# Kernel tuning notes

Measured on AMD Instinct MI355X. Metric: run time of the kernel, lower is better.

## Reference

```python
import jax, jax.numpy as jnp
import numpy as np

NUM_NODES = 100_000
NUM_EDGES = 3_200_000
THETA = 1.0  # module hyperparameter (default 1.0)


def setup_inputs() -> dict:
    key = jax.random.key(0)
    k_v, k_src, k_dst, k_t1, k_t2, k_r = jax.random.split(key, 6)
    v = jax.random.normal(k_v, (NUM_NODES,), dtype=jnp.float32)
    src = jax.random.randint(k_src, (NUM_EDGES,), 0, NUM_NODES, dtype=jnp.int32)
    dst = jax.random.randint(k_dst, (NUM_EDGES,), 0, NUM_NODES, dtype=jnp.int32)
    theta_sd_1 = jax.random.normal(k_t1, (NUM_EDGES,), dtype=jnp.float32) * 0.1
    theta_sd_2 = jax.random.normal(k_t2, (NUM_EDGES,), dtype=jnp.float32) * 0.1
    # conductance = 1/resistance, resistance in (0.5, 2.0) -> conductance in (0.5, 2.0)
    conductance = 1.0 / jax.random.uniform(k_r, (NUM_EDGES,), dtype=jnp.float32, minval=0.5, maxval=2.0)
    return {"t": 0, "v": v, "src": src, "dst": dst,
            "theta_sd_1": theta_sd_1, "theta_sd_2": theta_sd_2,
            "conductance": conductance}


def reference(t, v, src, dst, theta_sd_1, theta_sd_2, conductance):
    # per-edge gated current: g(vs, vd) = relu(theta1*(vs - vd) + theta2)
    diff = v[src] - v[dst]                                   # [E]
    current = conductance * jax.nn.relu(theta_sd_1 * diff + theta_sd_2)  # [E]
    incoming = jax.ops.segment_sum(current, dst, num_segments=NUM_NODES)  # [N]
    outgoing = jax.ops.segment_sum(current, src, num_segments=NUM_NODES)  # [N]
    return (incoming - outgoing) / THETA
```

## Files before the change

kernel.cpp:

```cpp
#include <hip/hip_runtime.h>
#include <hip/hip_fp16.h>


#define TL        13
#define TILE      (1 << TL)
#define NTILES    13
#define NBINS     (NTILES * NTILES)
#define PA_BLK    1024
#define PA_EPT    4
#define PA_EPB    (PA_BLK * PA_EPT)
#define SCAPL     56
#define NREP      8
#define CURSTRIDE 16
#define PC_BLK    1024
#define S_PC      3
#define NCOPY     (2 * NTILES * S_PC)

typedef int      vi4 __attribute__((ext_vector_type(4)));
typedef float    vf4 __attribute__((ext_vector_type(4)));
typedef unsigned vu2 __attribute__((ext_vector_type(2)));

__device__ __forceinline__ unsigned f16b(float f) {
    return (unsigned)__half_as_ushort(__float2half(f));
}
__device__ __forceinline__ float f16v(unsigned u) {
    return __half2float(__ushort_as_half((unsigned short)(u & 0xFFFFu)));
}

__global__ __launch_bounds__(PA_BLK) void pa_kernel(
    const int*   __restrict__ src,
    const int*   __restrict__ dst,
    const float* __restrict__ t1,
    const float* __restrict__ t2,
    const float* __restrict__ cond,
    vu2*         __restrict__ recs,
    int*         __restrict__ cursors,
    int E, int SEGCAP)
{
    __shared__ vu2 sbuf[NBINS][SCAPL];
    __shared__ int scnt[NBINS];
    __shared__ int gbase[NBINS];

    for (int i = threadIdx.x; i < NBINS; i += PA_BLK) scnt[i] = 0;
    __syncthreads();

    const int i0 = blockIdx.x * PA_EPB + (int)threadIdx.x * PA_EPT;

    #define PUT(S, D, T1, T2, C)                                              \
        {                                                                     \
            int bin = ((S) >> TL) * NTILES + ((D) >> TL);                     \
            vu2 rec;                                                          \
            rec.x = (((unsigned)(D) & (TILE - 1)) << TL) |                    \
                    ((unsigned)(S) & (TILE - 1));                             \
            rec.y = (f16b((C) * (T1)) << 16) | f16b((C) * (T2));              \
            int idx = atomicAdd(&scnt[bin], 1);                               \
            if (idx < SCAPL) sbuf[bin][idx] = rec;                            \
        }

    if (i0 + PA_EPT <= E) {
        vi4 s4 = __builtin_nontemporal_load((const vi4*)(src  + i0));
        vi4 d4 = __builtin_nontemporal_load((const vi4*)(dst  + i0));
        vf4 a4 = __builtin_nontemporal_load((const vf4*)(t1   + i0));
        vf4 b4 = __builtin_nontemporal_load((const vf4*)(t2   + i0));
        vf4 c4 = __builtin_nontemporal_load((const vf4*)(cond + i0));
        PUT(s4.x, d4.x, a4.x, b4.x, c4.x)
        PUT(s4.y, d4.y, a4.y, b4.y, c4.y)
        PUT(s4.z, d4.z, a4.z, b4.z, c4.z)
        PUT(s4.w, d4.w, a4.w, b4.w, c4.w)
    } else {
        for (int i = i0; i < E && i < i0 + PA_EPT; ++i)
            PUT(src[i], dst[i], t1[i], t2[i], cond[i])
    }
    #undef PUT

    __syncthreads();
    const int rep = blockIdx.x & (NREP - 1);
    if (threadIdx.x < NBINS) {
        int c = min(scnt[threadIdx.x], SCAPL);
        int b = atomicAdd(&cursors[(threadIdx.x * NREP + rep) * CURSTRIDE], c);
        if (b > SEGCAP) b = SEGCAP;
        if (b + c > SEGCAP) c = SEGCAP - b;
        scnt[threadIdx.x]  = c;
        gbase[threadIdx.x] = b;
    }
    __syncthreads();

    const int wave = threadIdx.x >> 6;
    const int lane = threadIdx.x & 63;
    for (int r = wave; r < NBINS; r += (PA_BLK / 64)) {
        const int c = scnt[r];
        vu2* g = recs + (size_t)(r * NREP + rep) * SEGCAP + gbase[r];
        for (int j = lane; j < c; j += 64) g[j] = sbuf[r][j];
    }
}

__global__ __launch_bounds__(PC_BLK) void pc_kernel(
    const float* __restrict__ v,
    const vu2*   __restrict__ recs,
    const int*   __restrict__ cursors,
    float*       __restrict__ part,
    int N, int SEGCAP)
{
    __shared__ __align__(16) float tS[TILE];
    __shared__ __align__(16) float tD[TILE];
    __shared__ __align__(16) float aS[TILE];
    __shared__ __align__(16) float aD[TILE];

    const int bin = blockIdx.x / S_PC;
    const int s   = blockIdx.x % S_PC;
    const int sb  = bin / NTILES;
    const int db  = bin % NTILES;
    const int baseS = sb << TL;
    const int baseD = db << TL;
    const int lenS = min(TILE, N - baseS);
    const int lenD = min(TILE, N - baseD);

    for (int i = threadIdx.x; i < TILE; i += PC_BLK) {
        tS[i] = (i < lenS) ? v[baseS + i] : 0.0f;
        tD[i] = (i < lenD) ? v[baseD + i] : 0.0f;
        aS[i] = 0.0f;
        aD[i] = 0.0f;
    }
    __syncthreads();

    for (int rep = 0; rep < NREP; ++rep) {
        const int cnt = min(cursors[(bin * NREP + rep) * CURSTRIDE], SEGCAP);
        const int j0  = (int)((long long)cnt * s       / S_PC);
        const int j1  = (int)((long long)cnt * (s + 1) / S_PC);
        const vu2* p  = recs + (size_t)(bin * NREP + rep) * SEGCAP;
        for (int j = j0 + (int)threadIdx.x; j < j1; j += PC_BLK) {
            vu2 r = p[j];
            const int   sl = (int)(r.x & (TILE - 1));
            const int   dl = (int)((r.x >> TL) & (TILE - 1));
            const float A  = f16v(r.y >> 16);
            const float B  = f16v(r.y);
            const float x  = fmaf(A, tS[sl] - tD[dl], B);
            if (x > 0.0f) {
                atomicAdd(&aS[sl], -x);
                atomicAdd(&aD[dl],  x);
            }
        }
    }
    __syncthreads();

    if (lenS > 0) {
        float* p = part + (size_t)(db * S_PC + s) * N + baseS;
        const int l4 = lenS & ~3;
        for (int i = (int)threadIdx.x * 4; i < l4; i += PC_BLK * 4)
            *(float4*)(p + i) = *(const float4*)&aS[i];
        for (int i = l4 + (int)threadIdx.x; i < lenS; i += PC_BLK)
            p[i] = aS[i];
    }
    if (lenD > 0) {
        float* p = part + (size_t)(NTILES * S_PC + sb * S_PC + s) * N + baseD;
        const int l4 = lenD & ~3;
        for (int i = (int)threadIdx.x * 4; i < l4; i += PC_BLK * 4)
            *(float4*)(p + i) = *(const float4*)&aD[i];
        for (int i = l4 + (int)threadIdx.x; i < lenD; i += PC_BLK)
            p[i] = aD[i];
    }
}

__global__ __launch_bounds__(256) void pe_kernel(
    const float* __restrict__ part, float* __restrict__ out, int N4)
{
    int n = blockIdx.x * blockDim.x + threadIdx.x;
    if (n < N4) {
        float4 sm = make_float4(0.f, 0.f, 0.f, 0.f);
        for (int c = 0; c < NCOPY; ++c) {
            float4 q = ((const float4*)part)[(size_t)c * N4 + n];
            sm.x += q.x; sm.y += q.y; sm.z += q.z; sm.w += q.w;
        }
        ((float4*)out)[n] = sm;
    }
}

__global__ __launch_bounds__(256) void pe_scalar_kernel(
    const float* __restrict__ part, float* __restrict__ out, int N)
{
    int n = blockIdx.x * blockDim.x + threadIdx.x;
    if (n < N) {
        float sm = 0.0f;
        for (int c = 0; c < NCOPY; ++c) sm += part[(size_t)c * N + n];
        out[n] = sm;
    }
}

__global__ __launch_bounds__(256) void atomic_fallback_kernel(
    const float* __restrict__ v, const int* __restrict__ src, const int* __restrict__ dst,
    const float* __restrict__ t1, const float* __restrict__ t2, const float* __restrict__ cond,
    float* __restrict__ out, int E)
{
    int i = blockIdx.x * blockDim.x + threadIdx.x;
    int stride = gridDim.x * blockDim.x;
    for (; i < E; i += stride) {
        int s = src[i], d = dst[i];
        float x = fmaf(t1[i], v[s] - v[d], t2[i]);
        if (x > 0.0f) {
            float c = cond[i] * x;
            atomicAdd(&out[d], c);
            atomicAdd(&out[s], -c);
        }
    }
}

extern "C" void kernel_launch(void* const* d_in, const int* in_sizes, int n_in,
                              void* d_out, int out_size, void* d_ws, size_t ws_size,
                              hipStream_t stream) {
    const float* v    = (const float*)d_in[1];
    const int*   src  = (const int*)  d_in[2];
    const int*   dst  = (const int*)  d_in[3];
    const float* t1   = (const float*)d_in[4];
    const float* t2   = (const float*)d_in[5];
    const float* cond = (const float*)d_in[6];
    float* out = (float*)d_out;
    const int E = in_sizes[2];
    const int N = out_size;

    const int segMean = E / (NBINS * NREP);
    const int SEGCAP  = ((segMean + segMean / 4 + 512) + 15) & ~15;

    const size_t recBytes = (size_t)NBINS * NREP * SEGCAP * sizeof(vu2);
    const size_t curBytes = (size_t)NBINS * NREP * CURSTRIDE * sizeof(int);
    const size_t parBytes = (size_t)NCOPY * N * sizeof(float);

    const bool ok = (N <= NTILES * TILE) && (E > 0) &&
                    (recBytes + curBytes + parBytes <= ws_size);

    if (ok) {
        vu2*   recs    = (vu2*)d_ws;
        int*   cursors = (int*)((char*)d_ws + recBytes);
        float* part    = (float*)((char*)d_ws + recBytes + curBytes);

        (void)hipMemsetAsync(cursors, 0, curBytes, stream);

        const int G = (E + PA_EPB - 1) / PA_EPB;
        pa_kernel<<<G, PA_BLK, 0, stream>>>(src, dst, t1, t2, cond,
                                            recs, cursors, E, SEGCAP);

        pc_kernel<<<NBINS * S_PC, PC_BLK, 0, stream>>>(v, recs, cursors, part,
                                                       N, SEGCAP);

        if ((N & 3) == 0) {
            const int N4 = N / 4;
            pe_kernel<<<(N4 + 255) / 256, 256, 0, stream>>>(part, out, N4);
        } else {
            pe_scalar_kernel<<<(N + 255) / 256, 256, 0, stream>>>(part, out, N);
        }
    } else {
        (void)hipMemsetAsync(out, 0, (size_t)N * sizeof(float), stream);
        int grid = (E + 255) / 256;
        if (grid > 2048) grid = 2048;
        atomic_fallback_kernel<<<grid, 256, 0, stream>>>(v, src, dst, t1, t2, cond, out, E);
    }
}
```

Measured before the change: 73.36 us.

## Fuse partition, compute and reduce into one cooperative persistent kernel

Replaces the memset and the three separate kernels (partition, per-bin compute, final reduction) with one cooperative kernel of 256 persistent blocks. The phases are separated by grid-wide syncs, and a single 128KB static LDS buffer is reused across phases. The aim is to remove launch and inter-kernel gaps. In exchange, each CU now runs only one block in every phase, the compute phase takes two rounds of bins per block, and the grid syncs add their own cost.

```diff
diff --git a/kernel.cpp b/kernel.cpp
--- a/kernel.cpp
+++ b/kernel.cpp
@@ -1,20 +1,23 @@
 #include <hip/hip_runtime.h>
 #include <hip/hip_fp16.h>
-
+#include <hip/hip_cooperative_groups.h>
+
+
+namespace cg = cooperative_groups;
 
 #define TL        13
 #define TILE      (1 << TL)
 #define NTILES    13
 #define NBINS     (NTILES * NTILES)
-#define PA_BLK    1024
-#define PA_EPT    4
-#define PA_EPB    (PA_BLK * PA_EPT)
+#define BLK       1024
+#define EPT       4
+#define EPB       (BLK * EPT)
 #define SCAPL     56
 #define NREP      8
 #define CURSTRIDE 16
-#define PC_BLK    1024
 #define S_PC      3
 #define NCOPY     (2 * NTILES * S_PC)
+#define NBLOCKS   256
 
 typedef int      vi4 __attribute__((ext_vector_type(4)));
 typedef float    vf4 __attribute__((ext_vector_type(4)));
@@ -27,7 +30,8 @@
     return __half2float(__ushort_as_half((unsigned short)(u & 0xFFFFu)));
 }
 
-__global__ __launch_bounds__(PA_BLK) void pa_kernel(
+__global__ __launch_bounds__(BLK) void fused_kernel(
+    const float* __restrict__ v,
     const int*   __restrict__ src,
     const int*   __restrict__ dst,
     const float* __restrict__ t1,
@@ -35,154 +39,168 @@
     const float* __restrict__ cond,
     vu2*         __restrict__ recs,
     int*         __restrict__ cursors,
-    int E, int SEGCAP)
+    float*       __restrict__ part,
+    float*       __restrict__ out,
+    int E, int N, int SEGCAP)
 {
-    __shared__ vu2 sbuf[NBINS][SCAPL];
+    cg::grid_group grid = cg::this_grid();
+
+    __shared__ __align__(16) unsigned char lds[131072];
     __shared__ int scnt[NBINS];
     __shared__ int gbase[NBINS];
 
-    for (int i = threadIdx.x; i < NBINS; i += PA_BLK) scnt[i] = 0;
-    __syncthreads();
-
-    const int i0 = blockIdx.x * PA_EPB + (int)threadIdx.x * PA_EPT;
-
-    #define PUT(S, D, T1, T2, C)                                              \
-        {                                                                     \
-            int bin = ((S) >> TL) * NTILES + ((D) >> TL);                     \
-            vu2 rec;                                                          \
-            rec.x = (((unsigned)(D) & (TILE - 1)) << TL) |                    \
-                    ((unsigned)(S) & (TILE - 1));                             \
-            rec.y = (f16b((C) * (T1)) << 16) | f16b((C) * (T2));              \
-            int idx = atomicAdd(&scnt[bin], 1);                               \
-            if (idx < SCAPL) sbuf[bin][idx] = rec;                            \
-        }
-
-    if (i0 + PA_EPT <= E) {
-        vi4 s4 = __builtin_nontemporal_load((const vi4*)(src  + i0));
-        vi4 d4 = __builtin_nontemporal_load((const vi4*)(dst  + i0));
-        vf4 a4 = __builtin_nontemporal_load((const vf4*)(t1   + i0));
-        vf4 b4 = __builtin_nontemporal_load((const vf4*)(t2   + i0));
-        vf4 c4 = __builtin_nontemporal_load((const vf4*)(cond + i0));
-        PUT(s4.x, d4.x, a4.x, b4.x, c4.x)
-        PUT(s4.y, d4.y, a4.y, b4.y, c4.y)
-        PUT(s4.z, d4.z, a4.z, b4.z, c4.z)
-        PUT(s4.w, d4.w, a4.w, b4.w, c4.w)
-    } else {
-        for (int i = i0; i < E && i < i0 + PA_EPT; ++i)
-            PUT(src[i], dst[i], t1[i], t2[i], cond[i])
-    }
-    #undef PUT
-
-    __syncthreads();
-    const int rep = blockIdx.x & (NREP - 1);
-    if (threadIdx.x < NBINS) {
-        int c = min(scnt[threadIdx.x], SCAPL);
-        int b = atomicAdd(&cursors[(threadIdx.x * NREP + rep) * CURSTRIDE], c);
-        if (b > SEGCAP) b = SEGCAP;
-        if (b + c > SEGCAP) c = SEGCAP - b;
-        scnt[threadIdx.x]  = c;
-        gbase[threadIdx.x] = b;
-    }
-    __syncthreads();
-
-    const int wave = threadIdx.x >> 6;
-    const int lane = threadIdx.x & 63;
-    for (int r = wave; r < NBINS; r += (PA_BLK / 64)) {
-        const int c = scnt[r];
-        vu2* g = recs + (size_t)(r * NREP + rep) * SEGCAP + gbase[r];
-        for (int j = lane; j < c; j += 64) g[j] = sbuf[r][j];
-    }
-}
-
-__global__ __launch_bounds__(PC_BLK) void pc_kernel(
-    const float* __restrict__ v,
-    const vu2*   __restrict__ recs,
-    const int*   __restrict__ cursors,
-    float*       __restrict__ part,
-    int N, int SEGCAP)
-{
-    __shared__ __align__(16) float tS[TILE];
-    __shared__ __align__(16) float tD[TILE];
-    __shared__ __align__(16) float aS[TILE];
-    __shared__ __align__(16) float aD[TILE];
-
-    const int bin = blockIdx.x / S_PC;
-    const int s   = blockIdx.x % S_PC;
-    const int sb  = bin / NTILES;
-    const int db  = bin % NTILES;
-    const int baseS = sb << TL;
-    const int baseD = db << TL;
-    const int lenS = min(TILE, N - baseS);
-    const int lenD = min(TILE, N - baseD);
-
-    for (int i = threadIdx.x; i < TILE; i += PC_BLK) {
-        tS[i] = (i < lenS) ? v[baseS + i] : 0.0f;
-        tD[i] = (i < lenD) ? v[baseD + i] : 0.0f;
-        aS[i] = 0.0f;
-        aD[i] = 0.0f;
-    }
-    __syncthreads();
-
-    for (int rep = 0; rep < NREP; ++rep) {
-        const int cnt = min(cursors[(bin * NREP + rep) * CURSTRIDE], SEGCAP);
-        const int j0  = (int)((long long)cnt * s       / S_PC);
-        const int j1  = (int)((long long)cnt * (s + 1) / S_PC);
-        const vu2* p  = recs + (size_t)(bin * NREP + rep) * SEGCAP;
-        for (int j = j0 + (int)threadIdx.x; j < j1; j += PC_BLK) {
-            vu2 r = p[j];
-            const int   sl = (int)(r.x & (TILE - 1));
-            const int   dl = (int)((r.x >> TL) & (TILE - 1));
-            const float A  = f16v(r.y >> 16);
-            const float B  = f16v(r.y);
-            const float x  = fmaf(A, tS[sl] - tD[dl], B);
-            if (x > 0.0f) {
-                atomicAdd(&aS[sl], -x);
-                atomicAdd(&aD[dl],  x);
-            }
-        }
-    }
-    __syncthreads();
-
-    if (lenS > 0) {
-        float* p = part + (size_t)(db * S_PC + s) * N + baseS;
-        const int l4 = lenS & ~3;
-        for (int i = (int)threadIdx.x * 4; i < l4; i += PC_BLK * 4)
-            *(float4*)(p + i) = *(const float4*)&aS[i];
-        for (int i = l4 + (int)threadIdx.x; i < lenS; i += PC_BLK)
-            p[i] = aS[i];
-    }
-    if (lenD > 0) {
-        float* p = part + (size_t)(NTILES * S_PC + sb * S_PC + s) * N + baseD;
-        const int l4 = lenD & ~3;
-        for (int i = (int)threadIdx.x * 4; i < l4; i += PC_BLK * 4)
-            *(float4*)(p + i) = *(const float4*)&aD[i];
-        for (int i = l4 + (int)threadIdx.x; i < lenD; i += PC_BLK)
-            p[i] = aD[i];
-    }
-}
-
-__global__ __launch_bounds__(256) void pe_kernel(
-    const float* __restrict__ part, float* __restrict__ out, int N4)
-{
-    int n = blockIdx.x * blockDim.x + threadIdx.x;
-    if (n < N4) {
-        float4 sm = make_float4(0.f, 0.f, 0.f, 0.f);
-        for (int c = 0; c < NCOPY; ++c) {
-            float4 q = ((const float4*)part)[(size_t)c * N4 + n];
-            sm.x += q.x; sm.y += q.y; sm.z += q.z; sm.w += q.w;
-        }
-        ((float4*)out)[n] = sm;
-    }
-}
-
-__global__ __launch_bounds__(256) void pe_scalar_kernel(
-    const float* __restrict__ part, float* __restrict__ out, int N)
-{
-    int n = blockIdx.x * blockDim.x + threadIdx.x;
-    if (n < N) {
-        float sm = 0.0f;
-        for (int c = 0; c < NCOPY; ++c) sm += part[(size_t)c * N + n];
-        out[n] = sm;
+    {
+        const int total = NBINS * NREP * CURSTRIDE;
+        const int idx = blockIdx.x * BLK + (int)threadIdx.x;
+        if (idx < total) cursors[idx] = 0;
+    }
+    grid.sync();
+
+    {
+        vu2 (*sbuf)[SCAPL] = (vu2(*)[SCAPL])lds;
+        const int G = (E + EPB - 1) / EPB;
+
+        for (int chunk = blockIdx.x; chunk < G; chunk += NBLOCKS) {
+            for (int i = threadIdx.x; i < NBINS; i += BLK) scnt[i] = 0;
+            __syncthreads();
+
+            const int i0 = chunk * EPB + (int)threadIdx.x * EPT;
+
+            #define PUT(S, D, T1, T2, C)                                          \
+                {                                                                 \
+                    int bin = ((S) >> TL) * NTILES + ((D) >> TL);                 \
+                    vu2 rec;                                                      \
+                    rec.x = (((unsigned)(D) & (TILE - 1)) << TL) |                \
+                            ((unsigned)(S) & (TILE - 1));                         \
+                    rec.y = (f16b((C) * (T1)) << 16) | f16b((C) * (T2));          \
+                    int idx = atomicAdd(&scnt[bin], 1);                           \
+                    if (idx < SCAPL) sbuf[bin][idx] = rec;                        \
+                }
+
+            if (i0 + EPT <= E) {
+                vi4 s4 = __builtin_nontemporal_load((const vi4*)(src  + i0));
+                vi4 d4 = __builtin_nontemporal_load((const vi4*)(dst  + i0));
+                vf4 a4 = __builtin_nontemporal_load((const vf4*)(t1   + i0));
+                vf4 b4 = __builtin_nontemporal_load((const vf4*)(t2   + i0));
+                vf4 c4 = __builtin_nontemporal_load((const vf4*)(cond + i0));
+                PUT(s4.x, d4.x, a4.x, b4.x, c4.x)
+                PUT(s4.y, d4.y, a4.y, b4.y, c4.y)
+                PUT(s4.z, d4.z, a4.z, b4.z, c4.z)
+                PUT(s4.w, d4.w, a4.w, b4.w, c4.w)
+            } else {
+                for (int i = i0; i < E && i < i0 + EPT; ++i)
+                    PUT(src[i], dst[i], t1[i], t2[i], cond[i])
+            }
+            #undef PUT
+
+            __syncthreads();
+            const int rep = chunk & (NREP - 1);
+            if (threadIdx.x < NBINS) {
+                int c = min(scnt[threadIdx.x], SCAPL);
+                int b = atomicAdd(&cursors[(threadIdx.x * NREP + rep) * CURSTRIDE], c);
+                if (b > SEGCAP) b = SEGCAP;
+                if (b + c > SEGCAP) c = SEGCAP - b;
+                scnt[threadIdx.x]  = c;
+                gbase[threadIdx.x] = b;
+            }
+            __syncthreads();
+
+            const int wave = threadIdx.x >> 6;
+            const int lane = threadIdx.x & 63;
+            for (int r = wave; r < NBINS; r += (BLK / 64)) {
+                const int c = scnt[r];
+                vu2* g = recs + (size_t)(r * NREP + rep) * SEGCAP + gbase[r];
+                if (lane < c) g[lane] = sbuf[r][lane];
+            }
+            __syncthreads();
+        }
+    }
+    grid.sync();
+
+    {
+        float* tS = (float*)lds;
+        float* tD = tS + TILE;
+        float* aS = tD + TILE;
+        float* aD = aS + TILE;
+
+        const int NWORK = NBINS * S_PC;
+        for (int w = blockIdx.x; w < NWORK; w += NBLOCKS) {
+            const int bin = w / S_PC;
+            const int s   = w - bin * S_PC;
+            const int sb  = bin / NTILES;
+            const int db  = bin - sb * NTILES;
+            const int baseS = sb << TL;
+            const int baseD = db << TL;
+            const int lenS = min(TILE, N - baseS);
+            const int lenD = min(TILE, N - baseD);
+
+            for (int i = threadIdx.x; i < TILE; i += BLK) {
+                tS[i] = (i < lenS) ? v[baseS + i] : 0.0f;
+                tD[i] = (i < lenD) ? v[baseD + i] : 0.0f;
+                aS[i] = 0.0f;
+                aD[i] = 0.0f;
+            }
+            __syncthreads();
+
+            for (int rep = 0; rep < NREP; ++rep) {
+                const int cnt = min(cursors[(bin * NREP + rep) * CURSTRIDE], SEGCAP);
+                const int j0  = (int)((long long)cnt * s       / S_PC);
+                const int j1  = (int)((long long)cnt * (s + 1) / S_PC);
+                const vu2* p  = recs + (size_t)(bin * NREP + rep) * SEGCAP;
+                for (int j = j0 + (int)threadIdx.x; j < j1; j += BLK) {
+                    vu2 r = p[j];
+                    const int   sl = (int)(r.x & (TILE - 1));
+                    const int   dl = (int)((r.x >> TL) & (TILE - 1));
+                    const float A  = f16v(r.y >> 16);
+                    const float B  = f16v(r.y);
+                    const float x  = fmaf(A, tS[sl] - tD[dl], B);
+                    if (x > 0.0f) {
+                        atomicAdd(&aS[sl], -x);
+                        atomicAdd(&aD[dl],  x);
+                    }
+                }
+            }
+            __syncthreads();
+
+            if (lenS > 0) {
+                float* p = part + (size_t)(db * S_PC + s) * N + baseS;
+                const int l4 = lenS & ~3;
+                for (int i = (int)threadIdx.x * 4; i < l4; i += BLK * 4)
+                    *(float4*)(p + i) = *(const float4*)&aS[i];
+                for (int i = l4 + (int)threadIdx.x; i < lenS; i += BLK)
+                    p[i] = aS[i];
+            }
+            if (lenD > 0) {
+                float* p = part + (size_t)(NTILES * S_PC + sb * S_PC + s) * N + baseD;
+                const int l4 = lenD & ~3;
+                for (int i = (int)threadIdx.x * 4; i < l4; i += BLK * 4)
+                    *(float4*)(p + i) = *(const float4*)&aD[i];
+                for (int i = l4 + (int)threadIdx.x; i < lenD; i += BLK)
+                    p[i] = aD[i];
+            }
+            __syncthreads();
+        }
+    }
+    grid.sync();
+
+    {
+        const int tid = blockIdx.x * BLK + (int)threadIdx.x;
+        const int nthreads = NBLOCKS * BLK;
+        if ((N & 3) == 0) {
+            const int N4 = N >> 2;
+            for (int n = tid; n < N4; n += nthreads) {
+                vf4 sm = (vf4)(0.0f);
+                for (int c = 0; c < NCOPY; ++c)
+                    sm += ((const vf4*)part)[(size_t)c * N4 + n];
+                ((vf4*)out)[n] = sm;
+            }
+        } else {
+            for (int n = tid; n < N; n += nthreads) {
+                float sm = 0.0f;
+                for (int c = 0; c < NCOPY; ++c) sm += part[(size_t)c * N + n];
+                out[n] = sm;
+            }
+        }
     }
 }
 
@@ -232,21 +250,13 @@
         int*   cursors = (int*)((char*)d_ws + recBytes);
         float* part    = (float*)((char*)d_ws + recBytes + curBytes);
 
-        (void)hipMemsetAsync(cursors, 0, curBytes, stream);
-
-        const int G = (E + PA_EPB - 1) / PA_EPB;
-        pa_kernel<<<G, PA_BLK, 0, stream>>>(src, dst, t1, t2, cond,
-                                            recs, cursors, E, SEGCAP);
-
-        pc_kernel<<<NBINS * S_PC, PC_BLK, 0, stream>>>(v, recs, cursors, part,
-                                                       N, SEGCAP);
-
-        if ((N & 3) == 0) {
-            const int N4 = N / 4;
-            pe_kernel<<<(N4 + 255) / 256, 256, 0, stream>>>(part, out, N4);
-        } else {
-            pe_scalar_kernel<<<(N + 255) / 256, 256, 0, stream>>>(part, out, N);
-        }
+        void* args[] = { (void*)&v, (void*)&src, (void*)&dst, (void*)&t1,
+                         (void*)&t2, (void*)&cond, (void*)&recs, (void*)&cursors,
+                         (void*)&part, (void*)&out,
+                         (void*)&E, (void*)&N, (void*)&SEGCAP };
+        (void)hipLaunchCooperativeKernel((void*)fused_kernel,
+                                         dim3(NBLOCKS), dim3(BLK),
+                                         args, 0, stream);
     } else {
         (void)hipMemsetAsync(out, 0, (size_t)N * sizeof(float), stream);
         int grid = (E + 255) / 256;
```

Result: slower. 172.0 us (+134.5%).
